# Kernel optimization log

Hardware: AMD Instinct MI355X
Metric: run time of the kernel (lower is better)

The kernel has to match this reference:

```python
import jax, jax.numpy as jnp
import numpy as np

B, C, H, W = 2, 64, 256, 256
DN = ('NCHW', 'OIHW', 'NCHW')


def _conv1x1(x, w, b):
    # x: [B,C,H,W], w: [O,C,1,1]
    return jnp.einsum('bchw,oc->bohw', x, w[:, :, 0, 0]) + b[None, :, None, None]


def _dw3x3(x, w, b):
    # depthwise 3x3, padding=1, groups=C; w: [C,1,3,3]
    y = jax.lax.conv_general_dilated(x, w, (1, 1), [(1, 1), (1, 1)],
                                     feature_group_count=x.shape[1],
                                     dimension_numbers=DN)
    return y + b[None, :, None, None]


def _proj(x, w1, b1, w2, b2):
    return _dw3x3(_conv1x1(x, w1, b1), w2, b2)


def _pixel_attention(initial, pattn1, pa_w, pa_b):
    b, c, h, w = initial.shape
    # interleave channels: [x_c0, p_c0, x_c1, p_c1, ...] per 'b c t h w -> b (c t) h w'
    x2 = jnp.stack([initial, pattn1], axis=2).reshape(b, 2 * c, h, w)
    x2 = jnp.pad(x2, ((0, 0), (0, 0), (3, 3), (3, 3)), mode='reflect')
    y = jax.lax.conv_general_dilated(x2, pa_w, (1, 1), 'VALID',
                                     feature_group_count=c,
                                     dimension_numbers=DN)
    return jax.nn.sigmoid(y + pa_b[None, :, None, None])


def setup_inputs() -> dict:
    key = jax.random.key(0)
    ks = jax.random.split(key, 26)

    def n(k, shape, s=0.05):
        return jax.random.normal(k, shape, dtype=jnp.float32) * s

    d = {
        'x_l': jax.random.normal(ks[0], (B, C, H, W), dtype=jnp.float32),
        'x_r': jax.random.normal(ks[1], (B, C, H, W), dtype=jnp.float32),
    }
    i = 2
    for pfx in ('lp1', 'rp1', 'lp2', 'rp2'):
        d[pfx + '_w1'] = n(ks[i], (C, C, 1, 1)); i += 1
        d[pfx + '_b1'] = n(ks[i], (C,)); i += 1
        d[pfx + '_w2'] = n(ks[i], (C, 1, 3, 3)); i += 1
        d[pfx + '_b2'] = n(ks[i], (C,)); i += 1
    for pfx in ('lp3', 'rp3'):
        d[pfx + '_w'] = n(ks[i], (C, C, 1, 1)); i += 1
        d[pfx + '_b'] = n(ks[i], (C,)); i += 1
    d['pa_w'] = n(ks[i], (C, 2, 7, 7)); i += 1
    d['pa_b'] = n(ks[i], (C,))
    return d


def reference(x_l, x_r,
              lp1_w1, lp1_b1, lp1_w2, lp1_b2,
              rp1_w1, rp1_b1, rp1_w2, rp1_b2,
              lp2_w1, lp2_b1, lp2_w2, lp2_b2,
              rp2_w1, rp2_b1, rp2_w2, rp2_b2,
              lp3_w, lp3_b, rp3_w, rp3_b,
              pa_w, pa_b):
    c = x_l.shape[1]
    scale = c ** (-0.5)
    initial = x_l + x_r

    # projections (1x1 conv + depthwise 3x3), then move channels last: [B,H,W,C]
    Q_l = _proj(x_l, lp1_w1, lp1_b1, lp1_w2, lp1_b2).transpose(0, 2, 3, 1)
    Q_r = _proj(x_r, rp1_w1, rp1_b1, rp1_w2, rp1_b2).transpose(0, 2, 3, 1)
    V_l = _proj(x_l, lp2_w1, lp2_b1, lp2_w2, lp2_b2).transpose(0, 2, 3, 1)
    V_r = _proj(x_r, rp2_w1, rp2_b1, rp2_w2, rp2_b2).transpose(0, 2, 3, 1)

    # cross-attention along the width axis per spatial row: [B,H,W,W]
    attn = jnp.einsum('bhwc,bhvc->bhwv', Q_l, Q_r) * scale
    F_r2l = jnp.einsum('bhwv,bhvc->bhwc', jax.nn.softmax(attn, axis=-1), V_r)
    F_l2r = jnp.einsum('bhwv,bhwc->bhvc', jax.nn.softmax(attn, axis=2), V_l)

    F_r2l = _conv1x1(F_r2l.transpose(0, 3, 1, 2), lp3_w, lp3_b)
    F_l2r = _conv1x1(F_l2r.transpose(0, 3, 1, 2), rp3_w, rp3_b)

    # PixelAttention returns sigmoid(...); EAGFM applies sigmoid again (faithful)
    a = jax.nn.sigmoid(_pixel_attention(initial, F_l2r + F_r2l, pa_w, pa_b))
    return a * x_l + (1.0 - a) * x_r
```

## Files before the change

kernel.cpp:

```cpp
#include <hip/hip_runtime.h>

typedef unsigned int uint;
typedef unsigned short ushort;
typedef _Float16 h2 __attribute__((ext_vector_type(2)));
typedef _Float16 f16x8 __attribute__((ext_vector_type(8)));
typedef float f32x4 __attribute__((ext_vector_type(4)));

#define HW 65536
#define W_ 256
#define H_ 256
#define C_ 64

__device__ __forceinline__ ushort f2hu(float f) { union { ushort u; _Float16 h; } x; x.h = (_Float16)f; return x.u; }
__device__ __forceinline__ float hu2f(ushort u) { union { ushort u; _Float16 h; } x; x.u = u; return (float)x.h; }

#define MFMA16(a, b, c) __builtin_amdgcn_mfma_f32_16x16x32_f16((a), (b), (c), 0, 0, 0)

__global__ __launch_bounds__(256) void wconv_k(const float* __restrict__ a0, const float* __restrict__ a1,
                                               const float* __restrict__ a2, const float* __restrict__ a3,
                                               const float* __restrict__ a4, const float* __restrict__ a5,
                                               ushort* __restrict__ dst) {
    int m = blockIdx.x;
    const float* src = m == 0 ? a0 : m == 1 ? a1 : m == 2 ? a2 : m == 3 ? a3 : m == 4 ? a4 : a5;
    ushort* d = dst + m * 4096;
    for (int i = threadIdx.x; i < 4096; i += 256) d[i] = f2hu(src[i]);
}

__global__ __launch_bounds__(256) void wpat_k(const float* __restrict__ pw, ushort* __restrict__ tbl) {
    int c = blockIdx.x;
    for (int i = threadIdx.x; i < 7168; i += 256) {
        int j = i & 7;
        int lane = (i >> 3) & 63;
        int f = i >> 9;
        int arr = f < 7 ? 0 : 1;
        int dy = f < 7 ? f : f - 7;
        int l15 = lane & 15, quad = lane >> 4;
        int k = quad * 8 + j;
        int t = k - l15 - 1;
        float v = (t >= 0 && t < 7) ? pw[c * 98 + arr * 49 + dy * 7 + t] : 0.0f;
        tbl[c * 7168 + i] = f2hu(v);
    }
}

__global__ __launch_bounds__(256, 2) void c1df_k(const float* __restrict__ xl,
                                                 const float* __restrict__ xr,
                                                 const ushort* __restrict__ wf16,
                                                 const float* __restrict__ bA0, const float* __restrict__ bB0,
                                                 const float* __restrict__ bA1, const float* __restrict__ bB1,
                                                 ushort* __restrict__ y0A, ushort* __restrict__ y0B,
                                                 ushort* __restrict__ y1A, ushort* __restrict__ y1B) {
    __shared__ ushort sS[64 * 268];
    int side = blockIdx.y;
    const float* x = side ? xr : xl;
    const ushort* wfA = wf16 + side * 4096;
    const ushort* wfB = wf16 + (2 + side) * 4096;
    const float* biasA = side ? bA1 : bA0;
    const float* biasB = side ? bB1 : bB0;
    ushort* yAo = side ? y1A : y0A;
    ushort* yBo = side ? y1B : y0B;

    int tid = threadIdx.x;
    int wv = tid >> 6, lane = tid & 63;
    int l15 = lane & 15, quad = lane >> 4;
    int pix0 = blockIdx.x * 256;
    int b = pix0 >> 16, hw0 = pix0 & 65535;
    const float* xb = x + ((size_t)b << 22) + hw0;

#pragma unroll
    for (int i = 0; i < 16; ++i) {
        int idx = i * 256 + tid;
        int cc = idx >> 6;
        int p4 = idx & 63;
        float4 v = *(const float4*)(xb + ((size_t)cc << 16) + p4 * 4);
        uint2 pk;
        pk.x = (uint)f2hu(v.x) | ((uint)f2hu(v.y) << 16);
        pk.y = (uint)f2hu(v.z) | ((uint)f2hu(v.w) << 16);
        *(uint2*)&sS[cc * 268 + p4 * 4] = pk;
    }
    __syncthreads();

    f16x8 aX[4][2];
#pragma unroll
    for (int mt = 0; mt < 4; ++mt) {
        int pixl = wv * 64 + mt * 16 + l15;
#pragma unroll
        for (int kc = 0; kc < 2; ++kc) {
            f16x8 a;
#pragma unroll
            for (int j = 0; j < 8; ++j) {
                int c = kc * 32 + quad * 8 + j;
                a[j] = *(const _Float16*)&sS[c * 268 + pixl];
            }
            aX[mt][kc] = a;
        }
    }

    for (int mat = 0; mat < 2; ++mat) {
        const ushort* wf = mat == 0 ? wfA : wfB;
        const float* bias = mat == 0 ? biasA : biasB;
        ushort* y = mat == 0 ? yAo : yBo;

        f16x8 bW[4][2];
#pragma unroll
        for (int nt = 0; nt < 4; ++nt)
#pragma unroll
            for (int kc = 0; kc < 2; ++kc)
                bW[nt][kc] = *(const f16x8*)(wf + (nt * 16 + l15) * 64 + kc * 32 + quad * 8);

        f32x4 acc[4][4];
#pragma unroll
        for (int mt = 0; mt < 4; ++mt)
#pragma unroll
            for (int nt = 0; nt < 4; ++nt) {
                f32x4 s = (f32x4)(0.0f);
                s = MFMA16(aX[mt][0], bW[nt][0], s);
                s = MFMA16(aX[mt][1], bW[nt][1], s);
                acc[mt][nt] = s;
            }

        __syncthreads();
#pragma unroll
        for (int nt = 0; nt < 4; ++nt) {
            int o = nt * 16 + l15;
            float bv = bias[o];
#pragma unroll
            for (int mt = 0; mt < 4; ++mt) {
                int pixl = wv * 64 + mt * 16 + quad * 4;
#pragma unroll
                for (int r = 0; r < 4; r += 2) {
                    h2 hh;
                    hh.x = (_Float16)(acc[mt][nt][r] + bv);
                    hh.y = (_Float16)(acc[mt][nt][r + 1] + bv);
                    *(h2*)&sS[o * 268 + pixl + r] = hh;
                }
            }
        }
        __syncthreads();
        ushort* yb = y + ((((size_t)b << 16) + hw0 + tid) << 6);
#pragma unroll
        for (int g = 0; g < 8; ++g) {
            ushort vs[8];
#pragma unroll
            for (int k = 0; k < 8; ++k) vs[k] = sS[(g * 8 + k) * 268 + tid];
            uint4 o;
            o.x = (uint)vs[0] | ((uint)vs[1] << 16);
            o.y = (uint)vs[2] | ((uint)vs[3] << 16);
            o.z = (uint)vs[4] | ((uint)vs[5] << 16);
            o.w = (uint)vs[6] | ((uint)vs[7] << 16);
            *(uint4*)(yb + g * 8) = o;
        }
    }
}

__global__ __launch_bounds__(256) void dwq2_k(const ushort* __restrict__ x0, const ushort* __restrict__ x1,
                                              const float* __restrict__ w0, const float* __restrict__ w1,
                                              const float* __restrict__ b0, const float* __restrict__ b1,
                                              ushort* __restrict__ o0, ushort* __restrict__ o1) {
    int z = blockIdx.z;
    int side = z >> 1, b = z & 1;
    const ushort* xcl = side ? x1 : x0;
    const float* wgt = side ? w1 : w0;
    const float* bias = side ? b1 : b0;
    ushort* out = side ? o1 : o0;
    __shared__ float sW[576];
    int tid = threadIdx.x;
    for (int i = tid; i < 576; i += 256) sW[i] = wgt[i];
    __syncthreads();
    int c = tid & 63, wq = tid >> 6;
    int wt = blockIdx.x, h0 = blockIdx.y * 4;
    int wbase = wt * 64 + wq * 16;
    const float* wp = sW + c * 9;
    float bv = bias[c];
    float acc[4][16];
#pragma unroll
    for (int o = 0; o < 4; ++o)
#pragma unroll
        for (int i = 0; i < 16; ++i) acc[o][i] = bv;
    size_t plane = (size_t)b << 16;
#pragma unroll
    for (int r = 0; r < 6; ++r) {
        int hh = h0 - 1 + r;
        int hhc = hh < 0 ? 0 : (hh > 255 ? 255 : hh);
        bool okh = (hh >= 0 && hh <= 255);
        float v[18];
#pragma unroll
        for (int t = 0; t < 18; ++t) {
            int ww = wbase - 1 + t;
            int wwc = ww < 0 ? 0 : (ww > 255 ? 255 : ww);
            float xv = hu2f(xcl[((plane + (size_t)hhc * 256 + wwc) << 6) + c]);
            v[t] = (okh && ww >= 0 && ww <= 255) ? xv : 0.0f;
        }
#pragma unroll
        for (int o = 0; o < 4; ++o) {
            if (o >= r - 2 && o <= r) {
                int wr = r - o;
                float wa = wp[wr * 3], wb = wp[wr * 3 + 1], wc2 = wp[wr * 3 + 2];
#pragma unroll
                for (int i = 0; i < 16; ++i)
                    acc[o][i] += wa * v[i] + wb * v[i + 1] + wc2 * v[i + 2];
            }
        }
    }
#pragma unroll
    for (int o = 0; o < 4; ++o) {
        size_t obase = ((plane + (size_t)(h0 + o) * 256 + wbase) << 6) + c;
#pragma unroll
        for (int i = 0; i < 16; ++i)
            out[obase + ((size_t)i << 6)] = f2hu(acc[o][i]);
    }
}

__global__ __launch_bounds__(256) void dwv2_k(const ushort* __restrict__ x0, const ushort* __restrict__ x1,
                                              const float* __restrict__ w0, const float* __restrict__ w1,
                                              const float* __restrict__ b0, const float* __restrict__ b1,
                                              ushort* __restrict__ o0, ushort* __restrict__ o1) {
    int z = blockIdx.z;
    int side = z >> 1, b = z & 1;
    const ushort* xcl = side ? x1 : x0;
    const float* wgt = side ? w1 : w0;
    const float* bias = side ? b1 : b0;
    ushort* out = side ? o1 : o0;
    __shared__ float sW[576];
    __shared__ ushort sT[4][64 * 66];
    int tid = threadIdx.x;
    for (int i = tid; i < 576; i += 256) sW[i] = wgt[i];
    __syncthreads();
    int c = tid & 63, wq = tid >> 6;
    int wt = blockIdx.x, h0 = blockIdx.y * 4;
    int wbase = wt * 64 + wq * 16;
    const float* wp = sW + c * 9;
    float bv = bias[c];
    float acc[4][16];
#pragma unroll
    for (int o = 0; o < 4; ++o)
#pragma unroll
        for (int i = 0; i < 16; ++i) acc[o][i] = bv;
    size_t plane = (size_t)b << 16;
#pragma unroll
    for (int r = 0; r < 6; ++r) {
        int hh = h0 - 1 + r;
        int hhc = hh < 0 ? 0 : (hh > 255 ? 255 : hh);
        bool okh = (hh >= 0 && hh <= 255);
        float v[18];
#pragma unroll
        for (int t = 0; t < 18; ++t) {
            int ww = wbase - 1 + t;
            int wwc = ww < 0 ? 0 : (ww > 255 ? 255 : ww);
            float xv = hu2f(xcl[((plane + (size_t)hhc * 256 + wwc) << 6) + c]);
            v[t] = (okh && ww >= 0 && ww <= 255) ? xv : 0.0f;
        }
#pragma unroll
        for (int o = 0; o < 4; ++o) {
            if (o >= r - 2 && o <= r) {
                int wr = r - o;
                float wa = wp[wr * 3], wb = wp[wr * 3 + 1], wc2 = wp[wr * 3 + 2];
#pragma unroll
                for (int i = 0; i < 16; ++i)
                    acc[o][i] += wa * v[i] + wb * v[i + 1] + wc2 * v[i + 2];
            }
        }
    }
#pragma unroll
    for (int o = 0; o < 4; ++o)
#pragma unroll
        for (int i = 0; i < 16; i += 2) {
            h2 hh2;
            hh2.x = (_Float16)acc[o][i];
            hh2.y = (_Float16)acc[o][i + 1];
            *(h2*)&sT[o][c * 66 + wq * 16 + i] = hh2;
        }
    __syncthreads();
    int cr = tid >> 2, ch = tid & 3;
#pragma unroll
    for (int o = 0; o < 4; ++o) {
        uint vb[8];
#pragma unroll
        for (int k = 0; k < 8; ++k) vb[k] = *(const uint*)&sT[o][cr * 66 + ch * 16 + k * 2];
        uint4 q0, q1;
        q0.x = vb[0]; q0.y = vb[1]; q0.z = vb[2]; q0.w = vb[3];
        q1.x = vb[4]; q1.y = vb[5]; q1.z = vb[6]; q1.w = vb[7];
        size_t bh16 = ((size_t)b * 256 + h0 + o) * 16384;
        ushort* ob = out + bh16 + (size_t)cr * 256 + wt * 64 + ch * 16;
        *(uint4*)ob = q0;
        *(uint4*)(ob + 8) = q1;
    }
}

__global__ __launch_bounds__(256, 2) void att2_k(const ushort* __restrict__ Ql,
                                                 const ushort* __restrict__ Qr,
                                                 const ushort* __restrict__ Vl,
                                                 const ushort* __restrict__ Vr,
                                                 ushort* __restrict__ Fr2l,
                                                 ushort* __restrict__ Fl2r) {
    int bh = blockIdx.x;
    int tid = threadIdx.x;
    int wv = tid >> 6, lane = tid & 63;
    int l15 = lane & 15, quad = lane >> 4;
    __shared__ ushort sE[256 * 72];
    __shared__ ushort sEt[64 * 264];

    const ushort* qlb = Ql + (size_t)bh * 16384;
    const ushort* qrb = Qr + (size_t)bh * 16384;
    const ushort* vlb = Vl + (size_t)bh * 16384;
    const ushort* vrb = Vr + (size_t)bh * 16384;
    int p0 = wv * 64;
    int c0 = wv * 16;

    f16x8 aQ[4][2];
#pragma unroll
    for (int mt = 0; mt < 4; ++mt)
#pragma unroll
        for (int kc = 0; kc < 2; ++kc)
            aQ[mt][kc] = *(const f16x8*)(qlb + (p0 + mt * 16 + l15) * 64 + kc * 32 + quad * 8);

    f16x8 onesf;
#pragma unroll
    for (int i = 0; i < 8; ++i) onesf[i] = (_Float16)1.0f;

    f32x4 num1[4][4];
    f32x4 den[4];
#pragma unroll
    for (int mt = 0; mt < 4; ++mt) {
        den[mt] = (f32x4)(0.0f);
#pragma unroll
        for (int nt = 0; nt < 4; ++nt) num1[mt][nt] = (f32x4)(0.0f);
    }

    for (int kt = 0; kt < 4; ++kt) {
        int k0 = kt * 64;
        f32x4 S[4][4];
#pragma unroll
        for (int nt = 0; nt < 4; ++nt) {
            f16x8 bQ[2];
#pragma unroll
            for (int kc = 0; kc < 2; ++kc)
                bQ[kc] = *(const f16x8*)(qrb + (k0 + nt * 16 + l15) * 64 + kc * 32 + quad * 8);
#pragma unroll
            for (int mt = 0; mt < 4; ++mt) {
                f32x4 s = (f32x4)(0.0f);
                s = MFMA16(aQ[mt][0], bQ[0], s);
                s = MFMA16(aQ[mt][1], bQ[1], s);
                S[mt][nt] = s;
            }
        }
#pragma unroll
        for (int mt = 0; mt < 4; ++mt)
#pragma unroll
            for (int nt = 0; nt < 4; ++nt)
#pragma unroll
                for (int r = 0; r < 4; ++r)
                    S[mt][nt][r] = __expf(S[mt][nt][r] * 0.125f);

        __syncthreads();
#pragma unroll
        for (int mt = 0; mt < 4; ++mt)
#pragma unroll
            for (int nt = 0; nt < 4; ++nt)
#pragma unroll
                for (int r = 0; r < 4; ++r)
                    sE[(p0 + mt * 16 + quad * 4 + r) * 72 + nt * 16 + l15] = f2hu(S[mt][nt][r]);
#pragma unroll
        for (int mt = 0; mt < 4; ++mt)
#pragma unroll
            for (int nt = 0; nt < 4; ++nt)
#pragma unroll
            for (int pr = 0; pr < 4; pr += 2) {
                h2 hh;
                hh.x = (_Float16)S[mt][nt][pr];
                hh.y = (_Float16)S[mt][nt][pr + 1];
                *(h2*)&sEt[(nt * 16 + l15) * 264 + p0 + mt * 16 + quad * 4 + pr] = hh;
            }
        __syncthreads();

        f16x8 aE[4][2];
#pragma unroll
        for (int mt = 0; mt < 4; ++mt)
#pragma unroll
            for (int kc = 0; kc < 2; ++kc)
                aE[mt][kc] = *(const f16x8*)&sE[(p0 + mt * 16 + l15) * 72 + kc * 32 + quad * 8];
#pragma unroll
        for (int mt = 0; mt < 4; ++mt) {
            den[mt] = MFMA16(aE[mt][0], onesf, den[mt]);
            den[mt] = MFMA16(aE[mt][1], onesf, den[mt]);
        }
#pragma unroll
        for (int nt = 0; nt < 4; ++nt) {
            f16x8 bV[2];
#pragma unroll
            for (int kc = 0; kc < 2; ++kc)
                bV[kc] = *(const f16x8*)(vrb + (nt * 16 + l15) * 256 + k0 + kc * 32 + quad * 8);
#pragma unroll
            for (int mt = 0; mt < 4; ++mt) {
                num1[mt][nt] = MFMA16(aE[mt][0], bV[0], num1[mt][nt]);
                num1[mt][nt] = MFMA16(aE[mt][1], bV[1], num1[mt][nt]);
            }
        }
        f32x4 num2[4], den2[4];
#pragma unroll
        for (int mt = 0; mt < 4; ++mt) { num2[mt] = (f32x4)(0.0f); den2[mt] = (f32x4)(0.0f); }
        for (int pc = 0; pc < 8; ++pc) {
            f16x8 bL = *(const f16x8*)(vlb + (c0 + l15) * 256 + pc * 32 + quad * 8);
#pragma unroll
            for (int mt = 0; mt < 4; ++mt) {
                f16x8 aT = *(const f16x8*)&sEt[(mt * 16 + l15) * 264 + pc * 32 + quad * 8];
                num2[mt] = MFMA16(aT, bL, num2[mt]);
                den2[mt] = MFMA16(aT, onesf, den2[mt]);
            }
        }
#pragma unroll
        for (int mt = 0; mt < 4; ++mt)
#pragma unroll
            for (int r = 0; r < 4; ++r) {
                float v = num2[mt][r] * (1.0f / den2[mt][r]);
                Fl2r[(size_t)bh * 16384 + (k0 + mt * 16 + quad * 4 + r) * 64 + c0 + l15] = f2hu(v);
            }
    }
#pragma unroll
    for (int mt = 0; mt < 4; ++mt)
#pragma unroll
        for (int r = 0; r < 4; ++r) {
            float inv = 1.0f / den[mt][r];
#pragma unroll
            for (int nt = 0; nt < 4; ++nt) {
                float v = num1[mt][nt][r] * inv;
                Fr2l[(size_t)bh * 16384 + (p0 + mt * 16 + quad * 4 + r) * 64 + nt * 16 + l15] = f2hu(v);
            }
        }
}

__global__ __launch_bounds__(256, 2) void p3m_k(const ushort* __restrict__ F1,
                                                const ushort* __restrict__ F2,
                                                const ushort* __restrict__ wf1,
                                                const float* __restrict__ b1,
                                                const ushort* __restrict__ wf2,
                                                const float* __restrict__ b2,
                                                ushort* __restrict__ outp) {
    __shared__ ushort sY[64 * 264];
    int tid = threadIdx.x;
    int wv = tid >> 6, lane = tid & 63;
    int l15 = lane & 15, quad = lane >> 4;
    int pix0 = blockIdx.x * 256;
    int b = pix0 >> 16, hw0 = pix0 & 65535;

    f32x4 acc[4][4];
#pragma unroll
    for (int mt = 0; mt < 4; ++mt)
#pragma unroll
        for (int nt = 0; nt < 4; ++nt) acc[mt][nt] = (f32x4)(0.0f);

    for (int mat = 0; mat < 2; ++mat) {
        const ushort* F = mat == 0 ? F1 : F2;
        const ushort* wf = mat == 0 ? wf1 : wf2;
        f16x8 aF[4][2], bW[4][2];
#pragma unroll
        for (int mt = 0; mt < 4; ++mt) {
            int pixg = pix0 + wv * 64 + mt * 16 + l15;
#pragma unroll
            for (int kc = 0; kc < 2; ++kc)
                aF[mt][kc] = *(const f16x8*)(F + (size_t)pixg * 64 + kc * 32 + quad * 8);
        }
#pragma unroll
        for (int nt = 0; nt < 4; ++nt)
#pragma unroll
            for (int kc = 0; kc < 2; ++kc)
                bW[nt][kc] = *(const f16x8*)(wf + (nt * 16 + l15) * 64 + kc * 32 + quad * 8);
#pragma unroll
        for (int mt = 0; mt < 4; ++mt)
#pragma unroll
            for (int nt = 0; nt < 4; ++nt) {
                acc[mt][nt] = MFMA16(aF[mt][0], bW[nt][0], acc[mt][nt]);
                acc[mt][nt] = MFMA16(aF[mt][1], bW[nt][1], acc[mt][nt]);
            }
    }

#pragma unroll
    for (int nt = 0; nt < 4; ++nt) {
        int o = nt * 16 + l15;
        float bv = b1[o] + b2[o];
#pragma unroll
        for (int mt = 0; mt < 4; ++mt) {
            int pixl = wv * 64 + mt * 16 + quad * 4;
#pragma unroll
            for (int r = 0; r < 4; r += 2) {
                h2 hh;
                hh.x = (_Float16)(acc[mt][nt][r] + bv);
                hh.y = (_Float16)(acc[mt][nt][r + 1] + bv);
                *(h2*)&sY[o * 264 + pixl + r] = hh;
            }
        }
    }
    __syncthreads();
    ushort* yb = outp + ((size_t)b << 22) + hw0;
#pragma unroll
    for (int i = 0; i < 16; ++i) {
        int o = wv * 16 + i;
        uint2 v = *(const uint2*)&sY[o * 264 + lane * 4];
        *(uint2*)(yb + ((size_t)o << 16) + lane * 4) = v;
    }
}

__global__ __launch_bounds__(256, 4) void p4m_k(const float* __restrict__ x_l,
                                                const float* __restrict__ x_r,
                                                const ushort* __restrict__ pt,
                                                const ushort* __restrict__ tbl,
                                                const float* __restrict__ pb,
                                                float* __restrict__ out) {
    __shared__ ushort s_t[22 * 320];
    __shared__ ushort p_t[22 * 320];
    int tid = threadIdx.x;
    int tile = blockIdx.x & 15;
    int bc = blockIdx.x >> 4;
    int c = bc & 63;
    int h0 = tile << 4;
    size_t cbase = (size_t)bc << 16;

    {
        int a = tid & 127, rr = tid >> 7;
        int k = 2 * a + 4;
        int slotbase = (k >> 3);
        for (int pass = 0; pass < 11; ++pass) {
            int row = pass * 2 + rr;
            int hh = h0 + row - 3;
            hh = hh < 0 ? -hh : (hh > 255 ? 510 - hh : hh);
            size_t rb = cbase + ((size_t)hh << 8);
            float2 xl2 = *(const float2*)(x_l + rb + 2 * a);
            float2 xr2 = *(const float2*)(x_r + rb + 2 * a);
            uint pv = *(const uint*)(pt + rb + 2 * a);
            h2 sh;
            sh.x = (_Float16)(xl2.x + xr2.x);
            sh.y = (_Float16)(xl2.y + xr2.y);
            int off = row * 320 + (((slotbase ^ (row & 7)) << 3) | (k & 7));
            *(h2*)&s_t[off] = sh;
            *(uint*)&p_t[off] = pv;
        }
    }
    if (tid < 176) {
        int row = tid >> 3, g = tid & 7;
        int k = g < 2 ? g * 2 : (g < 4 ? 260 + (g - 2) * 2 : 264 + (g - 4) * 2);
        h2 sh; uint pv;
        if (g < 4) {
            int hh = h0 + row - 3;
            hh = hh < 0 ? -hh : (hh > 255 ? 510 - hh : hh);
            size_t rb = cbase + ((size_t)hh << 8);
            int w0 = k - 4, w1 = k - 3;
            int s0 = w0 < 0 ? -w0 : (w0 > 255 ? 510 - w0 : w0);
            int s1 = w1 < 0 ? -w1 : (w1 > 255 ? 510 - w1 : w1);
            sh.x = (_Float16)(x_l[rb + s0] + x_r[rb + s0]);
            sh.y = (_Float16)(x_l[rb + s1] + x_r[rb + s1]);
            pv = (uint)pt[rb + s0] | ((uint)pt[rb + s1] << 16);
        } else {
            sh.x = (_Float16)0.0f; sh.y = (_Float16)0.0f;
            pv = 0;
        }
        int off = row * 320 + ((((k >> 3) ^ (row & 7)) << 3) | (k & 7));
        *(h2*)&s_t[off] = sh;
        *(uint*)&p_t[off] = pv;
    }

    int wv = tid >> 6, lane = tid & 63;
    int l15 = lane & 15, quad = lane >> 4;
    const ushort* tb = tbl + c * 7168;
    f16x8 bW[14];
#pragma unroll
    for (int f = 0; f < 14; ++f)
        bW[f] = *(const f16x8*)(tb + (f * 64 + lane) * 8);

    float bias = pb[c];
    f32x4 acc[4];
#pragma unroll
    for (int t = 0; t < 4; ++t) acc[t] = (f32x4)(bias);

    __syncthreads();

#pragma unroll
    for (int f = 0; f < 14; ++f) {
        int dy = f < 7 ? f : f - 7;
        const ushort* tp = f < 7 ? s_t : p_t;
        int row = l15 + dy;
        int rbase = row * 320;
        int rx = row & 7;
#pragma unroll
        for (int t = 0; t < 4; ++t) {
            int L = wv * 8 + 2 * t + quad;
            f16x8 aF = *(const f16x8*)&tp[rbase + ((L ^ rx) << 3)];
            acc[t] = MFMA16(aF, bW[f], acc[t]);
        }
    }

    int hrow = h0 + quad * 4;
#pragma unroll
    for (int t = 0; t < 4; ++t) {
        int w = wv * 64 + t * 16 + l15;
#pragma unroll
        for (int r = 0; r < 4; ++r) {
            size_t idx = cbase + (size_t)(hrow + r) * 256 + w;
            float z = acc[t][r];
            float s1 = 1.0f / (1.0f + __expf(-z));
            float a  = 1.0f / (1.0f + __expf(-s1));
            float xl = x_l[idx], xr = x_r[idx];
            out[idx] = xr + a * (xl - xr);
        }
    }
}

extern "C" void kernel_launch(void* const* d_in, const int* in_sizes, int n_in,
                              void* d_out, int out_size, void* d_ws, size_t ws_size,
                              hipStream_t stream) {
    const float* x_l = (const float*)d_in[0];
    const float* x_r = (const float*)d_in[1];
    const float* lp1_w1 = (const float*)d_in[2];
    const float* lp1_b1 = (const float*)d_in[3];
    const float* lp1_w2 = (const float*)d_in[4];
    const float* lp1_b2 = (const float*)d_in[5];
    const float* rp1_w1 = (const float*)d_in[6];
    const float* rp1_b1 = (const float*)d_in[7];
    const float* rp1_w2 = (const float*)d_in[8];
    const float* rp1_b2 = (const float*)d_in[9];
    const float* lp2_w1 = (const float*)d_in[10];
    const float* lp2_b1 = (const float*)d_in[11];
    const float* lp2_w2 = (const float*)d_in[12];
    const float* lp2_b2 = (const float*)d_in[13];
    const float* rp2_w1 = (const float*)d_in[14];
    const float* rp2_b1 = (const float*)d_in[15];
    const float* rp2_w2 = (const float*)d_in[16];
    const float* rp2_b2 = (const float*)d_in[17];
    const float* lp3_w = (const float*)d_in[18];
    const float* lp3_b = (const float*)d_in[19];
    const float* rp3_w = (const float*)d_in[20];
    const float* rp3_b = (const float*)d_in[21];
    const float* pa_w = (const float*)d_in[22];
    const float* pa_b = (const float*)d_in[23];

    const size_t N = (size_t)2 * 64 * 256 * 256;
    char* ws = (char*)d_ws;
    ushort* clA0 = (ushort*)ws;
    ushort* wf16 = (ushort*)(ws + N * 2);
    ushort* tbl  = (ushort*)(ws + N * 2 + 6 * 4096 * 2);
    ushort* q_l   = (ushort*)(ws + N * 4);
    ushort* q_r   = q_l + N;
    ushort* v_l   = q_r + N;
    ushort* v_r   = v_l + N;
    ushort* f_r2l = v_r + N;
    ushort* f_l2r = f_r2l + N;
    ushort* clB0  = f_l2r + N;
    ushort* clA1  = clB0 + N;
    ushort* clB1  = clA1 + N;

    dim3 blk(256);
    dim3 g_c1(512, 2);
    dim3 g_dw(4, 64, 4);
    dim3 g_att(512);
    dim3 g_p3(512);
    dim3 g_p4(2048);

    wconv_k<<<6, blk, 0, stream>>>(lp1_w1, rp1_w1, lp2_w1, rp2_w1, lp3_w, rp3_w, wf16);
    wpat_k<<<64, blk, 0, stream>>>(pa_w, tbl);

    c1df_k<<<g_c1, blk, 0, stream>>>(x_l, x_r, wf16,
                                     lp1_b1, lp2_b1, rp1_b1, rp2_b1,
                                     clA0, clB0, clA1, clB1);
    dwq2_k<<<g_dw, blk, 0, stream>>>(clA0, clA1, lp1_w2, rp1_w2, lp1_b2, rp1_b2, q_l, q_r);
    dwv2_k<<<g_dw, blk, 0, stream>>>(clB0, clB1, lp2_w2, rp2_w2, lp2_b2, rp2_b2, v_l, v_r);

    att2_k<<<g_att, blk, 0, stream>>>(q_l, q_r, v_l, v_r, f_r2l, f_l2r);

    p3m_k<<<g_p3, blk, 0, stream>>>(f_r2l, f_l2r, wf16 + 4 * 4096, lp3_b, wf16 + 5 * 4096, rp3_b, clA0);

    p4m_k<<<g_p4, blk, 0, stream>>>(x_l, x_r, clA0, tbl, pa_b, (float*)d_out);
}
```

Before: 305.4 us.

## Split cross-attention into independent per-direction, per-row-tile blocks recomputing scores

The fused attention kernel computed the score matrix once per row and reused it for both softmax directions through a shared-memory transpose. It is replaced by a kernel launched on a 512x8 grid where each block handles one direction (left-to-right or right-to-left) and one 64-row tile. The transposed direction recomputes scores with Q_r and Q_l swapped. This adds parallelism, cuts per-block shared memory and registers, drops block-wide barriers and raises the occupancy hint to 4. The cost is computing the QK^T product and exponentials twice and reloading K and V tiles from global memory once per tile.

```diff
diff --git a/kernel.cpp b/kernel.cpp
--- a/kernel.cpp
+++ b/kernel.cpp
@@ -286,146 +286,76 @@
     }
 }
 
-__global__ __launch_bounds__(256, 2) void att2_k(const ushort* __restrict__ Ql,
+__global__ __launch_bounds__(256, 4) void attx_k(const ushort* __restrict__ Ql,
                                                  const ushort* __restrict__ Qr,
                                                  const ushort* __restrict__ Vl,
                                                  const ushort* __restrict__ Vr,
                                                  ushort* __restrict__ Fr2l,
                                                  ushort* __restrict__ Fl2r) {
+    __shared__ ushort sE[64 * 264];
     int bh = blockIdx.x;
+    int role = blockIdx.y >> 2;
+    int tile = blockIdx.y & 3;
+    const ushort* P = role ? Qr : Ql;
+    const ushort* K = role ? Ql : Qr;
+    const ushort* V = role ? Vl : Vr;
+    ushort* out = role ? Fl2r : Fr2l;
+
     int tid = threadIdx.x;
     int wv = tid >> 6, lane = tid & 63;
     int l15 = lane & 15, quad = lane >> 4;
-    __shared__ ushort sE[256 * 72];
-    __shared__ ushort sEt[64 * 264];
-
-    const ushort* qlb = Ql + (size_t)bh * 16384;
-    const ushort* qrb = Qr + (size_t)bh * 16384;
-    const ushort* vlb = Vl + (size_t)bh * 16384;
-    const ushort* vrb = Vr + (size_t)bh * 16384;
-    int p0 = wv * 64;
-    int c0 = wv * 16;
-
-    f16x8 aQ[4][2];
-#pragma unroll
-    for (int mt = 0; mt < 4; ++mt)
-#pragma unroll
-        for (int kc = 0; kc < 2; ++kc)
-            aQ[mt][kc] = *(const f16x8*)(qlb + (p0 + mt * 16 + l15) * 64 + kc * 32 + quad * 8);
+    size_t base = (size_t)bh * 16384;
+    int r0 = tile * 64 + wv * 16;
+
+    f16x8 aP[2];
+#pragma unroll
+    for (int kc = 0; kc < 2; ++kc)
+        aP[kc] = *(const f16x8*)(P + base + (size_t)(r0 + l15) * 64 + kc * 32 + quad * 8);
 
     f16x8 onesf;
 #pragma unroll
     for (int i = 0; i < 8; ++i) onesf[i] = (_Float16)1.0f;
 
-    f32x4 num1[4][4];
-    f32x4 den[4];
-#pragma unroll
-    for (int mt = 0; mt < 4; ++mt) {
-        den[mt] = (f32x4)(0.0f);
-#pragma unroll
-        for (int nt = 0; nt < 4; ++nt) num1[mt][nt] = (f32x4)(0.0f);
-    }
-
-    for (int kt = 0; kt < 4; ++kt) {
-        int k0 = kt * 64;
-        f32x4 S[4][4];
+    f32x4 num[4];
+    f32x4 den = (f32x4)(0.0f);
+#pragma unroll
+    for (int nc = 0; nc < 4; ++nc) num[nc] = (f32x4)(0.0f);
+
+    ushort* sEw = sE + wv * 16 * 264;
+
+    for (int t = 0; t < 4; ++t) {
+        int k0 = t * 64;
 #pragma unroll
         for (int nt = 0; nt < 4; ++nt) {
-            f16x8 bQ[2];
-#pragma unroll
-            for (int kc = 0; kc < 2; ++kc)
-                bQ[kc] = *(const f16x8*)(qrb + (k0 + nt * 16 + l15) * 64 + kc * 32 + quad * 8);
-#pragma unroll
-            for (int mt = 0; mt < 4; ++mt) {
-                f32x4 s = (f32x4)(0.0f);
-                s = MFMA16(aQ[mt][0], bQ[0], s);
-                s = MFMA16(aQ[mt][1], bQ[1], s);
-                S[mt][nt] = s;
-            }
-        }
-#pragma unroll
-        for (int mt = 0; mt < 4; ++mt)
-#pragma unroll
-            for (int nt = 0; nt < 4; ++nt)
-#pragma unroll
-                for (int r = 0; r < 4; ++r)
-                    S[mt][nt][r] = __expf(S[mt][nt][r] * 0.125f);
-
-        __syncthreads();
-#pragma unroll
-        for (int mt = 0; mt < 4; ++mt)
-#pragma unroll
-            for (int nt = 0; nt < 4; ++nt)
-#pragma unroll
-                for (int r = 0; r < 4; ++r)
-                    sE[(p0 + mt * 16 + quad * 4 + r) * 72 + nt * 16 + l15] = f2hu(S[mt][nt][r]);
-#pragma unroll
-        for (int mt = 0; mt < 4; ++mt)
-#pragma unroll
-            for (int nt = 0; nt < 4; ++nt)
-#pragma unroll
-            for (int pr = 0; pr < 4; pr += 2) {
-                h2 hh;
-                hh.x = (_Float16)S[mt][nt][pr];
-                hh.y = (_Float16)S[mt][nt][pr + 1];
-                *(h2*)&sEt[(nt * 16 + l15) * 264 + p0 + mt * 16 + quad * 4 + pr] = hh;
-            }
-        __syncthreads();
-
-        f16x8 aE[4][2];
-#pragma unroll
-        for (int mt = 0; mt < 4; ++mt)
-#pragma unroll
-            for (int kc = 0; kc < 2; ++kc)
-                aE[mt][kc] = *(const f16x8*)&sE[(p0 + mt * 16 + l15) * 72 + kc * 32 + quad * 8];
-#pragma unroll
-        for (int mt = 0; mt < 4; ++mt) {
-            den[mt] = MFMA16(aE[mt][0], onesf, den[mt]);
-            den[mt] = MFMA16(aE[mt][1], onesf, den[mt]);
-        }
-#pragma unroll
-        for (int nt = 0; nt < 4; ++nt) {
-            f16x8 bV[2];
-#pragma unroll
-            for (int kc = 0; kc < 2; ++kc)
-                bV[kc] = *(const f16x8*)(vrb + (nt * 16 + l15) * 256 + k0 + kc * 32 + quad * 8);
-#pragma unroll
-            for (int mt = 0; mt < 4; ++mt) {
-                num1[mt][nt] = MFMA16(aE[mt][0], bV[0], num1[mt][nt]);
-                num1[mt][nt] = MFMA16(aE[mt][1], bV[1], num1[mt][nt]);
-            }
-        }
-        f32x4 num2[4], den2[4];
-#pragma unroll
-        for (int mt = 0; mt < 4; ++mt) { num2[mt] = (f32x4)(0.0f); den2[mt] = (f32x4)(0.0f); }
-        for (int pc = 0; pc < 8; ++pc) {
-            f16x8 bL = *(const f16x8*)(vlb + (c0 + l15) * 256 + pc * 32 + quad * 8);
-#pragma unroll
-            for (int mt = 0; mt < 4; ++mt) {
-                f16x8 aT = *(const f16x8*)&sEt[(mt * 16 + l15) * 264 + pc * 32 + quad * 8];
-                num2[mt] = MFMA16(aT, bL, num2[mt]);
-                den2[mt] = MFMA16(aT, onesf, den2[mt]);
-            }
-        }
-#pragma unroll
-        for (int mt = 0; mt < 4; ++mt)
-#pragma unroll
-            for (int r = 0; r < 4; ++r) {
-                float v = num2[mt][r] * (1.0f / den2[mt][r]);
-                Fl2r[(size_t)bh * 16384 + (k0 + mt * 16 + quad * 4 + r) * 64 + c0 + l15] = f2hu(v);
-            }
-    }
-#pragma unroll
-    for (int mt = 0; mt < 4; ++mt)
-#pragma unroll
-        for (int r = 0; r < 4; ++r) {
-            float inv = 1.0f / den[mt][r];
-#pragma unroll
-            for (int nt = 0; nt < 4; ++nt) {
-                float v = num1[mt][nt][r] * inv;
-                Fr2l[(size_t)bh * 16384 + (p0 + mt * 16 + quad * 4 + r) * 64 + nt * 16 + l15] = f2hu(v);
-            }
-        }
+            f16x8 bK0 = *(const f16x8*)(K + base + (size_t)(k0 + nt * 16 + l15) * 64 + quad * 8);
+            f16x8 bK1 = *(const f16x8*)(K + base + (size_t)(k0 + nt * 16 + l15) * 64 + 32 + quad * 8);
+            f32x4 s = (f32x4)(0.0f);
+            s = MFMA16(aP[0], bK0, s);
+            s = MFMA16(aP[1], bK1, s);
+#pragma unroll
+            for (int r = 0; r < 4; ++r)
+                sEw[(quad * 4 + r) * 264 + nt * 16 + l15] = f2hu(__expf(s[r] * 0.125f));
+        }
+#pragma unroll
+        for (int kcc = 0; kcc < 2; ++kcc) {
+            f16x8 aE = *(const f16x8*)&sEw[l15 * 264 + kcc * 32 + quad * 8];
+            den = MFMA16(aE, onesf, den);
+#pragma unroll
+            for (int nc = 0; nc < 4; ++nc) {
+                f16x8 bV = *(const f16x8*)(V + base + (size_t)(nc * 16 + l15) * 256 + k0 + kcc * 32 + quad * 8);
+                num[nc] = MFMA16(aE, bV, num[nc]);
+            }
+        }
+    }
+
+#pragma unroll
+    for (int r = 0; r < 4; ++r) {
+        float inv = 1.0f / den[r];
+        int row = r0 + quad * 4 + r;
+#pragma unroll
+        for (int nc = 0; nc < 4; ++nc)
+            out[base + (size_t)row * 64 + nc * 16 + l15] = f2hu(num[nc][r] * inv);
+    }
 }
 
 __global__ __launch_bounds__(256, 2) void p3m_k(const ushort* __restrict__ F1,
@@ -649,7 +579,7 @@
     dim3 blk(256);
     dim3 g_c1(512, 2);
     dim3 g_dw(4, 64, 4);
-    dim3 g_att(512);
+    dim3 g_att(512, 8);
     dim3 g_p3(512);
     dim3 g_p4(2048);
 
@@ -662,7 +592,7 @@
     dwq2_k<<<g_dw, blk, 0, stream>>>(clA0, clA1, lp1_w2, rp1_w2, lp1_b2, rp1_b2, q_l, q_r);
     dwv2_k<<<g_dw, blk, 0, stream>>>(clB0, clB1, lp2_w2, rp2_w2, lp2_b2, rp2_b2, v_l, v_r);
 
-    att2_k<<<g_att, blk, 0, stream>>>(q_l, q_r, v_l, v_r, f_r2l, f_l2r);
+    attx_k<<<g_att, blk, 0, stream>>>(q_l, q_r, v_l, v_r, f_r2l, f_l2r);
 
     p3m_k<<<g_p3, blk, 0, stream>>>(f_r2l, f_l2r, wf16 + 4 * 4096, lp3_b, wf16 + 5 * 4096, rp3_b, clA0);
 
```

Result: slower. 389.6 us (+27.6%).
